# Kernel optimization log

Measured on AMD Instinct MI355X. Metric: run time of the kernel, lower is better.

## Reference

```python
import jax, jax.numpy as jnp
import numpy as np

B, S, V, H = 16, 256, 32, 256
LN_EPS = 1e-5


def setup_inputs() -> dict:
    key = jax.random.key(0)
    ks = jax.random.split(key, 8)
    sW = 1.0 / np.sqrt(H)
    return {
        "x": jax.random.normal(ks[0], (B, S, V, 1), jnp.float32),
        "W1": jax.random.normal(ks[1], (V, H), jnp.float32),          # linear1: input_size=1
        "b1": jax.random.normal(ks[2], (V, H), jnp.float32) * 0.1,
        "W2": jax.random.normal(ks[3], (V, H, H), jnp.float32) * sW,
        "b2": jax.random.normal(ks[4], (V, H), jnp.float32) * 0.1,
        "Wg": jax.random.normal(ks[5], (V, H, H), jnp.float32) * sW,
        "bg": jax.random.normal(ks[6], (V, H), jnp.float32) * 0.1,
        "gamma": jnp.ones((V, H), jnp.float32),
        "beta": jnp.zeros((V, H), jnp.float32),
        "Wa": jax.random.normal(ks[7], (H,), jnp.float32) * sW,
        "ba": jnp.zeros((1,), jnp.float32),
    }


def reference(x, W1, b1, W2, b2, Wg, bg, gamma, beta, Wa, ba):
    # Batched GRN over all variables at once (replaces the per-var Python loop).
    # x: [B,S,V,1]; linear1 with input_size=1 is a scalar-vector outer product.
    h = jax.nn.relu(x * W1 + b1)                                  # [B,S,V,H]
    h = jnp.einsum('bsvh,vhk->bsvk', h, W2) + b2                  # linear2
    gated = jax.nn.sigmoid(jnp.einsum('bsvh,vhk->bsvk', h, Wg) + bg) * h
    # residual is the raw scalar input (last dim 1), broadcast over H as in torch
    pre = x + gated                                               # [B,S,V,H]
    mu = jnp.mean(pre, axis=-1, keepdims=True)
    var = jnp.mean(jnp.square(pre - mu), axis=-1, keepdims=True)
    var_outputs = (pre - mu) * jax.lax.rsqrt(var + LN_EPS) * gamma + beta
    # softmax attention pooling over variables
    scores = jnp.einsum('bsvh,h->bsv', var_outputs, Wa) + ba[0]   # [B,S,V]
    attn = jax.nn.softmax(scores, axis=-1)[..., None]             # [B,S,V,1]
    vsn_out = jnp.sum(var_outputs * attn, axis=2)                 # [B,S,H]
    return vsn_out, attn
```

## Files before the change

### kernel.cpp

```cpp
#include <hip/hip_runtime.h>
#include <hip/hip_bf16.h>

typedef _Float16 f16;
typedef _Float16 f16x2 __attribute__((ext_vector_type(2)));
typedef _Float16 f16x4 __attribute__((ext_vector_type(4)));
typedef _Float16 f16x8 __attribute__((ext_vector_type(8)));
typedef float f32x4 __attribute__((ext_vector_type(4)));

#define T_TOK 4096
#define V_N 32
#define H_N 256
#define LN_EPS_F 1e-5f

union U4 { f16x4 h; int i[2]; };
union U8 { f16x8 h; int i[4]; };

__device__ __forceinline__ void gload16(const f16* g, f16* l) {
    __builtin_amdgcn_global_load_lds(
        (const __attribute__((address_space(1))) void*)g,
        (__attribute__((address_space(3))) void*)l, 16, 0, 0);
}

__global__ __launch_bounds__(256) void prep_transpose(
    const float* __restrict__ W2, const float* __restrict__ Wg,
    f16* __restrict__ W2t, f16* __restrict__ Wgt)
{
    __shared__ float tile[64][65];
    int bid = blockIdx.x;
    int w = bid >> 9;
    int rem = bid & 511;
    int v = rem >> 4;
    int kt = (rem >> 2) & 3;
    int nt = rem & 3;
    const float* src = w ? Wg : W2;
    f16* dst = w ? Wgt : W2t;
    const float* base = src + ((size_t)v * H_N + (size_t)kt * 64) * H_N + nt * 64;
    int tid = threadIdx.x;
    #pragma unroll
    for (int p = 0; p < 16; ++p) {
        int idx = p * 256 + tid;
        int r = idx >> 6, c = idx & 63;
        tile[r][c] = base[(size_t)r * H_N + c];
    }
    __syncthreads();
    f16* obase = dst + ((size_t)v * H_N + (size_t)nt * 64) * H_N + kt * 64;
    #pragma unroll
    for (int p = 0; p < 16; ++p) {
        int idx = p * 256 + tid;
        int r = idx >> 6, c = idx & 63;
        obase[(size_t)r * H_N + c] = (f16)tile[c][r];
    }
}

__global__ __launch_bounds__(256) void prep_w1(
    const float* __restrict__ W1, const float* __restrict__ b1,
    f16* __restrict__ W1h, f16* __restrict__ b1h)
{
    int i = blockIdx.x * 256 + threadIdx.x;
    W1h[i] = (f16)W1[i];
    b1h[i] = (f16)b1[i];
}

__global__ __launch_bounds__(256, 2) void fused_grn(
    const float* __restrict__ x,
    const f16* __restrict__ W1h, const f16* __restrict__ b1h,
    const f16* __restrict__ W2t, const float* __restrict__ b2,
    const f16* __restrict__ Wgt, const float* __restrict__ bg,
    const float* __restrict__ gamma, const float* __restrict__ beta,
    const float* __restrict__ Wa, const float* __restrict__ ba,
    f16* __restrict__ VO,
    float* __restrict__ scores)
{
    __shared__ f16 Wb[2][256 * 32];

    int bid = blockIdx.x;
    int xcd = bid & 7, rr = bid >> 3;
    int v  = (xcd << 2) + (rr >> 6);
    int mt = rr & 63;
    int tid = threadIdx.x;
    int w = tid >> 6, lane = tid & 63;
    int lo = lane & 15, hi = lane >> 4;
    int m = mt * 64 + w * 16 + lo;

    const f16* W2v = W2t + ((size_t)v << 16);
    const f16* Wgv = Wgt + ((size_t)v << 16);

    auto stage = [&](const f16* Wv, int kt, int buf) {
        int cs = (lane & 3) ^ ((lane >> 2) & 3) ^ ((lane >> 4) & 3);
        #pragma unroll
        for (int i = 0; i < 4; ++i) {
            int n = ((w * 4 + i) << 4) + (lane >> 2);
            gload16(Wv + ((size_t)n << 8) + (kt << 5) + (cs << 3),
                    &Wb[buf][(w * 4 + i) << 9]);
        }
    };

    float xs = x[(size_t)m * V_N + v];
    f16 xh = (f16)xs;
    f16x8 x8 = { xh, xh, xh, xh, xh, xh, xh, xh };

    f32x4 acc[16] = {};
    const int afbase = ((hi ^ (lo & 3) ^ ((lo >> 2) & 3)) << 3);

    stage(W2v, 0, 0);
    __syncthreads();

    #pragma unroll
    for (int kt = 0; kt < 8; ++kt) {
        if (kt < 7) stage(W2v, kt + 1, (kt + 1) & 1);
        else        stage(Wgv, 0, 0);
        const int k0 = (kt << 5) + (hi << 3);
        f16x8 w8 = *(const f16x8*)&W1h[(v << 8) + k0];
        f16x8 c8 = *(const f16x8*)&b1h[(v << 8) + k0];
        f16x8 hv = x8 * w8 + c8;
        #pragma unroll
        for (int j = 0; j < 8; ++j) hv[j] = hv[j] > (f16)0 ? hv[j] : (f16)0;
        #pragma unroll
        for (int nf = 0; nf < 16; ++nf) {
            f16x8 af = *(const f16x8*)&Wb[kt & 1][((nf * 16 + lo) << 5) + afbase];
            acc[nf] = __builtin_amdgcn_mfma_f32_16x16x32_f16(af, hv, acc[nf], 0, 0, 0);
        }
        __syncthreads();
    }

    int H2p[16][2];
    #pragma unroll
    for (int nf = 0; nf < 16; ++nf) {
        f32x4 b4 = *(const f32x4*)&b2[(v << 8) + nf * 16 + hi * 4];
        f32x4 h = acc[nf] + b4;
        U4 u; u.h = f16x4{ (f16)h[0], (f16)h[1], (f16)h[2], (f16)h[3] };
        H2p[nf][0] = u.i[0]; H2p[nf][1] = u.i[1];
        acc[nf] = f32x4{0.f, 0.f, 0.f, 0.f};
    }

    int iq0 = lo + ((((hi << 1))     & 3) << 4);
    int iq1 = lo + ((((hi << 1) | 1) & 3) << 4);
    bool hiB = (hi >> 1) != 0;
    #pragma unroll
    for (int kt = 0; kt < 8; ++kt) {
        if (kt < 7) stage(Wgv, kt + 1, (kt + 1) & 1);
        int A0 = H2p[2 * kt][0],     A1 = H2p[2 * kt][1];
        int B0 = H2p[2 * kt + 1][0], B1 = H2p[2 * kt + 1][1];
        int a0 = __shfl(A0, iq0), a1 = __shfl(A1, iq0);
        int a2 = __shfl(A0, iq1), a3 = __shfl(A1, iq1);
        int b0 = __shfl(B0, iq0), b1_ = __shfl(B1, iq0);
        int b2_ = __shfl(B0, iq1), b3 = __shfl(B1, iq1);
        U8 u;
        u.i[0] = hiB ? b0  : a0;
        u.i[1] = hiB ? b1_ : a1;
        u.i[2] = hiB ? b2_ : a2;
        u.i[3] = hiB ? b3  : a3;
        #pragma unroll
        for (int nf = 0; nf < 16; ++nf) {
            f16x8 af = *(const f16x8*)&Wb[kt & 1][((nf * 16 + lo) << 5) + afbase];
            acc[nf] = __builtin_amdgcn_mfma_f32_16x16x32_f16(af, u.h, acc[nf], 0, 0, 0);
        }
        if (kt < 7) __syncthreads();
    }

    float s = 0.f, q = 0.f;
    #pragma unroll
    for (int nf = 0; nf < 16; ++nf) {
        f32x4 bgv = *(const f32x4*)&bg[(v << 8) + nf * 16 + hi * 4];
        U4 u; u.i[0] = H2p[nf][0]; u.i[1] = H2p[nf][1];
        #pragma unroll
        for (int r = 0; r < 4; ++r) {
            float a = acc[nf][r] + bgv[r];
            float g = 1.f / (1.f + __expf(-a));
            float val = g * (float)u.h[r];
            acc[nf][r] = val;
            s += val; q += val * val;
        }
    }
    s += __shfl_xor(s, 16); s += __shfl_xor(s, 32);
    q += __shfl_xor(q, 16); q += __shfl_xor(q, 32);
    float mu  = s * (1.f / 256.f);
    float var = q * (1.f / 256.f) - mu * mu;
    float inv = rsqrtf(var + LN_EPS_F);

    float sp = 0.f;
    f16* VOr = VO + ((size_t)v * T_TOK + m) * H_N;
    #pragma unroll
    for (int nf = 0; nf < 16; ++nf) {
        int n0 = nf * 16 + hi * 4;
        f32x4 gm = *(const f32x4*)&gamma[(v << 8) + n0];
        f32x4 bt = *(const f32x4*)&beta[(v << 8) + n0];
        f32x4 wa = *(const f32x4*)&Wa[n0];
        f16x4 ov;
        #pragma unroll
        for (int r = 0; r < 4; ++r) {
            float o = (acc[nf][r] - mu) * inv * gm[r] + bt[r];
            sp += o * wa[r];
            ov[r] = (f16)o;
        }
        *(f16x4*)&VOr[n0] = ov;
    }
    sp += __shfl_xor(sp, 16); sp += __shfl_xor(sp, 32);
    if (hi == 0) scores[(size_t)m * V_N + v] = sp + ba[0];
}

__global__ __launch_bounds__(128) void pool(
    const f16* __restrict__ VO,
    const float* __restrict__ scores,
    float* __restrict__ out)
{
    int t = blockIdx.x, tid = threadIdx.x;
    __shared__ float sc[V_N];
    if (tid < V_N) sc[tid] = scores[t * V_N + tid];
    __syncthreads();
    float mx = -1e30f;
    #pragma unroll
    for (int v = 0; v < V_N; ++v) mx = fmaxf(mx, sc[v]);
    float e[V_N];
    float sum = 0.f;
    #pragma unroll
    for (int v = 0; v < V_N; ++v) { e[v] = __expf(sc[v] - mx); sum += e[v]; }
    float isum = 1.f / sum;
    float a0 = 0.f, a1 = 0.f;
    #pragma unroll
    for (int v = 0; v < V_N; ++v) {
        f16x2 vv = *(const f16x2*)&VO[((size_t)v * T_TOK + t) * H_N + tid * 2];
        float ww = e[v] * isum;
        a0 = fmaf((float)vv[0], ww, a0);
        a1 = fmaf((float)vv[1], ww, a1);
    }
    *(float2*)&out[(size_t)t * H_N + tid * 2] = make_float2(a0, a1);
    if (tid < V_N)
        out[(size_t)T_TOK * H_N + (size_t)t * V_N + tid] = e[tid] * isum;
}

extern "C" void kernel_launch(void* const* d_in, const int* in_sizes, int n_in,
                              void* d_out, int out_size, void* d_ws, size_t ws_size,
                              hipStream_t stream)
{
    const float* x     = (const float*)d_in[0];
    const float* W1    = (const float*)d_in[1];
    const float* b1    = (const float*)d_in[2];
    const float* W2    = (const float*)d_in[3];
    const float* b2    = (const float*)d_in[4];
    const float* Wg    = (const float*)d_in[5];
    const float* bg    = (const float*)d_in[6];
    const float* gamma = (const float*)d_in[7];
    const float* beta  = (const float*)d_in[8];
    const float* Wa    = (const float*)d_in[9];
    const float* ba    = (const float*)d_in[10];
    float* out = (float*)d_out;

    char* ws = (char*)d_ws;
    f16* W2t = (f16*)ws;
    f16* Wgt = (f16*)(ws + ((size_t)4 << 20));
    f16* VO  = (f16*)(ws + ((size_t)8 << 20));
    float* scores = (float*)(ws + ((size_t)72 << 20));
    f16* W1h = (f16*)(ws + ((size_t)72 << 20) + (512 << 10));
    f16* b1h = (f16*)(ws + ((size_t)72 << 20) + (528 << 10));

    prep_transpose<<<1024, 256, 0, stream>>>(W2, Wg, W2t, Wgt);
    prep_w1<<<32, 256, 0, stream>>>(W1, b1, W1h, b1h);
    fused_grn<<<2048, 256, 0, stream>>>(x, W1h, b1h, W2t, b2, Wgt, bg,
                                        gamma, beta, Wa, ba, VO, scores);
    pool<<<4096, 128, 0, stream>>>(VO, scores, out);
}
```

Baseline: 120.9 us.

## Switch fused GRN to 32x32x16 MFMA with 128-token tiles

Rewrites the fused GRN kernel to use 32x32x16 MFMA instructions instead of 16x16x32. Each wave now covers 32 tokens, so each block covers 128 tokens and the grid is halved, which doubles reuse of each staged weight tile. The LDS swizzle, the register-resident H2 repacking (now a single lane^32 shuffle) and the LayerNorm reductions are rewritten to match the new accumulator layout. The cost is fewer blocks in the grid and more accumulator and H2 registers per thread, which may hurt occupancy under the two-blocks-per-CU launch bound.

```diff
diff --git a/kernel.cpp b/kernel.cpp
--- a/kernel.cpp
+++ b/kernel.cpp
@@ -6,6 +6,7 @@
 typedef _Float16 f16x4 __attribute__((ext_vector_type(4)));
 typedef _Float16 f16x8 __attribute__((ext_vector_type(8)));
 typedef float f32x4 __attribute__((ext_vector_type(4)));
+typedef float f32x16 __attribute__((ext_vector_type(16)));
 
 #define T_TOK 4096
 #define V_N 32
@@ -75,22 +76,22 @@
 
     int bid = blockIdx.x;
     int xcd = bid & 7, rr = bid >> 3;
-    int v  = (xcd << 2) + (rr >> 6);
-    int mt = rr & 63;
+    int v  = (xcd << 2) + (rr >> 5);
+    int mt = rr & 31;
     int tid = threadIdx.x;
     int w = tid >> 6, lane = tid & 63;
-    int lo = lane & 15, hi = lane >> 4;
-    int m = mt * 64 + w * 16 + lo;
+    int col = lane & 31, h = lane >> 5;
+    int m = mt * 128 + w * 32 + col;
 
     const f16* W2v = W2t + ((size_t)v << 16);
     const f16* Wgv = Wgt + ((size_t)v << 16);
 
-    auto stage = [&](const f16* Wv, int kt, int buf) {
-        int cs = (lane & 3) ^ ((lane >> 2) & 3) ^ ((lane >> 4) & 3);
+    auto stage = [&](const f16* Wv, int s, int buf) {
+        int cs = (lane & 3) ^ ((lane >> 2) & 3);
         #pragma unroll
         for (int i = 0; i < 4; ++i) {
             int n = ((w * 4 + i) << 4) + (lane >> 2);
-            gload16(Wv + ((size_t)n << 8) + (kt << 5) + (cs << 3),
+            gload16(Wv + ((size_t)n << 8) + (s << 5) + (cs << 3),
                     &Wb[buf][(w * 4 + i) << 9]);
         }
     };
@@ -99,104 +100,128 @@
     f16 xh = (f16)xs;
     f16x8 x8 = { xh, xh, xh, xh, xh, xh, xh, xh };
 
-    f32x4 acc[16] = {};
-    const int afbase = ((hi ^ (lo & 3) ^ ((lo >> 2) & 3)) << 3);
+    f32x16 acc[8] = {};
+    const int rowoff = col << 5;
+    const int cxor = col & 3;
 
     stage(W2v, 0, 0);
     __syncthreads();
 
     #pragma unroll
-    for (int kt = 0; kt < 8; ++kt) {
-        if (kt < 7) stage(W2v, kt + 1, (kt + 1) & 1);
-        else        stage(Wgv, 0, 0);
-        const int k0 = (kt << 5) + (hi << 3);
-        f16x8 w8 = *(const f16x8*)&W1h[(v << 8) + k0];
-        f16x8 c8 = *(const f16x8*)&b1h[(v << 8) + k0];
-        f16x8 hv = x8 * w8 + c8;
-        #pragma unroll
-        for (int j = 0; j < 8; ++j) hv[j] = hv[j] > (f16)0 ? hv[j] : (f16)0;
-        #pragma unroll
-        for (int nf = 0; nf < 16; ++nf) {
-            f16x8 af = *(const f16x8*)&Wb[kt & 1][((nf * 16 + lo) << 5) + afbase];
-            acc[nf] = __builtin_amdgcn_mfma_f32_16x16x32_f16(af, hv, acc[nf], 0, 0, 0);
+    for (int s = 0; s < 8; ++s) {
+        if (s < 7) stage(W2v, s + 1, (s + 1) & 1);
+        else       stage(Wgv, 0, 0);
+        #pragma unroll
+        for (int t = 0; t < 2; ++t) {
+            const int kt = 2 * s + t;
+            const int k0 = (kt << 4) + (h << 3);
+            f16x8 w8 = *(const f16x8*)&W1h[(v << 8) + k0];
+            f16x8 c8 = *(const f16x8*)&b1h[(v << 8) + k0];
+            f16x8 hv = x8 * w8 + c8;
+            #pragma unroll
+            for (int j = 0; j < 8; ++j) hv[j] = hv[j] > (f16)0 ? hv[j] : (f16)0;
+            const int chunk = ((t << 1) + h) ^ cxor;
+            #pragma unroll
+            for (int nb = 0; nb < 8; ++nb) {
+                f16x8 af = *(const f16x8*)&Wb[s & 1][(nb << 10) + rowoff + (chunk << 3)];
+                acc[nb] = __builtin_amdgcn_mfma_f32_32x32x16_f16(af, hv, acc[nb], 0, 0, 0);
+            }
         }
         __syncthreads();
     }
 
-    int H2p[16][2];
-    #pragma unroll
-    for (int nf = 0; nf < 16; ++nf) {
-        f32x4 b4 = *(const f32x4*)&b2[(v << 8) + nf * 16 + hi * 4];
-        f32x4 h = acc[nf] + b4;
-        U4 u; u.h = f16x4{ (f16)h[0], (f16)h[1], (f16)h[2], (f16)h[3] };
-        H2p[nf][0] = u.i[0]; H2p[nf][1] = u.i[1];
-        acc[nf] = f32x4{0.f, 0.f, 0.f, 0.f};
-    }
-
-    int iq0 = lo + ((((hi << 1))     & 3) << 4);
-    int iq1 = lo + ((((hi << 1) | 1) & 3) << 4);
-    bool hiB = (hi >> 1) != 0;
-    #pragma unroll
-    for (int kt = 0; kt < 8; ++kt) {
-        if (kt < 7) stage(Wgv, kt + 1, (kt + 1) & 1);
-        int A0 = H2p[2 * kt][0],     A1 = H2p[2 * kt][1];
-        int B0 = H2p[2 * kt + 1][0], B1 = H2p[2 * kt + 1][1];
-        int a0 = __shfl(A0, iq0), a1 = __shfl(A1, iq0);
-        int a2 = __shfl(A0, iq1), a3 = __shfl(A1, iq1);
-        int b0 = __shfl(B0, iq0), b1_ = __shfl(B1, iq0);
-        int b2_ = __shfl(B0, iq1), b3 = __shfl(B1, iq1);
-        U8 u;
-        u.i[0] = hiB ? b0  : a0;
-        u.i[1] = hiB ? b1_ : a1;
-        u.i[2] = hiB ? b2_ : a2;
-        u.i[3] = hiB ? b3  : a3;
-        #pragma unroll
-        for (int nf = 0; nf < 16; ++nf) {
-            f16x8 af = *(const f16x8*)&Wb[kt & 1][((nf * 16 + lo) << 5) + afbase];
-            acc[nf] = __builtin_amdgcn_mfma_f32_16x16x32_f16(af, u.h, acc[nf], 0, 0, 0);
-        }
-        if (kt < 7) __syncthreads();
-    }
-
-    float s = 0.f, q = 0.f;
-    #pragma unroll
-    for (int nf = 0; nf < 16; ++nf) {
-        f32x4 bgv = *(const f32x4*)&bg[(v << 8) + nf * 16 + hi * 4];
-        U4 u; u.i[0] = H2p[nf][0]; u.i[1] = H2p[nf][1];
-        #pragma unroll
-        for (int r = 0; r < 4; ++r) {
-            float a = acc[nf][r] + bgv[r];
-            float g = 1.f / (1.f + __expf(-a));
-            float val = g * (float)u.h[r];
-            acc[nf][r] = val;
-            s += val; q += val * val;
-        }
-    }
-    s += __shfl_xor(s, 16); s += __shfl_xor(s, 32);
-    q += __shfl_xor(q, 16); q += __shfl_xor(q, 32);
-    float mu  = s * (1.f / 256.f);
-    float var = q * (1.f / 256.f) - mu * mu;
+    int H2i[64];
+    #pragma unroll
+    for (int nb = 0; nb < 8; ++nb) {
+        #pragma unroll
+        for (int p = 0; p < 4; ++p) {
+            int n0 = (nb << 5) + (p << 3) + (h << 2);
+            f32x4 b4 = *(const f32x4*)&b2[(v << 8) + n0];
+            U4 u;
+            u.h = f16x4{ (f16)(acc[nb][4 * p + 0] + b4[0]),
+                         (f16)(acc[nb][4 * p + 1] + b4[1]),
+                         (f16)(acc[nb][4 * p + 2] + b4[2]),
+                         (f16)(acc[nb][4 * p + 3] + b4[3]) };
+            H2i[nb * 8 + 2 * p]     = u.i[0];
+            H2i[nb * 8 + 2 * p + 1] = u.i[1];
+        }
+        #pragma unroll
+        for (int e = 0; e < 16; ++e) acc[nb][e] = 0.f;
+    }
+
+    #pragma unroll
+    for (int s = 0; s < 8; ++s) {
+        if (s < 7) stage(Wgv, s + 1, (s + 1) & 1);
+        #pragma unroll
+        for (int t = 0; t < 2; ++t) {
+            const int b = s * 8 + 4 * t;
+            int S0 = h ? H2i[b]     : H2i[b + 2];
+            int S1 = h ? H2i[b + 1] : H2i[b + 3];
+            int T0 = h ? H2i[b + 2] : H2i[b];
+            int T1 = h ? H2i[b + 3] : H2i[b + 1];
+            int R0 = __shfl(S0, lane ^ 32);
+            int R1 = __shfl(S1, lane ^ 32);
+            U8 u;
+            u.i[0] = h ? R0 : T0;
+            u.i[1] = h ? R1 : T1;
+            u.i[2] = h ? T0 : R0;
+            u.i[3] = h ? T1 : R1;
+            const int chunk = ((t << 1) + h) ^ cxor;
+            #pragma unroll
+            for (int nb = 0; nb < 8; ++nb) {
+                f16x8 af = *(const f16x8*)&Wb[s & 1][(nb << 10) + rowoff + (chunk << 3)];
+                acc[nb] = __builtin_amdgcn_mfma_f32_32x32x16_f16(af, u.h, acc[nb], 0, 0, 0);
+            }
+        }
+        if (s < 7) __syncthreads();
+    }
+
+    float sr = 0.f, qr = 0.f;
+    #pragma unroll
+    for (int nb = 0; nb < 8; ++nb) {
+        #pragma unroll
+        for (int p = 0; p < 4; ++p) {
+            int n0 = (nb << 5) + (p << 3) + (h << 2);
+            f32x4 bgv = *(const f32x4*)&bg[(v << 8) + n0];
+            U4 u2; u2.i[0] = H2i[nb * 8 + 2 * p]; u2.i[1] = H2i[nb * 8 + 2 * p + 1];
+            #pragma unroll
+            for (int r = 0; r < 4; ++r) {
+                float a = acc[nb][4 * p + r] + bgv[r];
+                float g = 1.f / (1.f + __expf(-a));
+                float val = g * (float)u2.h[r];
+                acc[nb][4 * p + r] = val;
+                sr += val; qr += val * val;
+            }
+        }
+    }
+    sr += __shfl_xor(sr, 32);
+    qr += __shfl_xor(qr, 32);
+    float mu  = sr * (1.f / 256.f);
+    float var = qr * (1.f / 256.f) - mu * mu;
     float inv = rsqrtf(var + LN_EPS_F);
 
     float sp = 0.f;
     f16* VOr = VO + ((size_t)v * T_TOK + m) * H_N;
     #pragma unroll
-    for (int nf = 0; nf < 16; ++nf) {
-        int n0 = nf * 16 + hi * 4;
-        f32x4 gm = *(const f32x4*)&gamma[(v << 8) + n0];
-        f32x4 bt = *(const f32x4*)&beta[(v << 8) + n0];
-        f32x4 wa = *(const f32x4*)&Wa[n0];
-        f16x4 ov;
-        #pragma unroll
-        for (int r = 0; r < 4; ++r) {
-            float o = (acc[nf][r] - mu) * inv * gm[r] + bt[r];
-            sp += o * wa[r];
-            ov[r] = (f16)o;
-        }
-        *(f16x4*)&VOr[n0] = ov;
-    }
-    sp += __shfl_xor(sp, 16); sp += __shfl_xor(sp, 32);
-    if (hi == 0) scores[(size_t)m * V_N + v] = sp + ba[0];
+    for (int nb = 0; nb < 8; ++nb) {
+        #pragma unroll
+        for (int p = 0; p < 4; ++p) {
+            int n0 = (nb << 5) + (p << 3) + (h << 2);
+            f32x4 gm = *(const f32x4*)&gamma[(v << 8) + n0];
+            f32x4 bt = *(const f32x4*)&beta[(v << 8) + n0];
+            f32x4 wa = *(const f32x4*)&Wa[n0];
+            f16x4 ov;
+            #pragma unroll
+            for (int r = 0; r < 4; ++r) {
+                float o = (acc[nb][4 * p + r] - mu) * inv * gm[r] + bt[r];
+                sp += o * wa[r];
+                ov[r] = (f16)o;
+            }
+            *(f16x4*)&VOr[n0] = ov;
+        }
+    }
+    sp += __shfl_xor(sp, 32);
+    if (h == 0) scores[(size_t)m * V_N + v] = sp + ba[0];
 }
 
 __global__ __launch_bounds__(128) void pool(
@@ -256,7 +281,7 @@
 
     prep_transpose<<<1024, 256, 0, stream>>>(W2, Wg, W2t, Wgt);
     prep_w1<<<32, 256, 0, stream>>>(W1, b1, W1h, b1h);
-    fused_grn<<<2048, 256, 0, stream>>>(x, W1h, b1h, W2t, b2, Wgt, bg,
+    fused_grn<<<1024, 256, 0, stream>>>(x, W1h, b1h, W2t, b2, Wgt, bg,
                                         gamma, beta, Wa, ba, VO, scores);
     pool<<<4096, 128, 0, stream>>>(VO, scores, out);
 }
```

New measurement: 144.7 us. 19.7% more time.
